# Kernel tuning notes

Hardware: AMD Instinct MI355X
Metric: run time of the kernel (lower is better)

Reference implementation:

```python
import jax, jax.numpy as jnp
import numpy as np

B, N, D = 8, 2048, 768


def setup_inputs() -> dict:
    key = jax.random.key(0)
    ks = jax.random.split(key, 12)
    s = 1.0 / np.sqrt(D)
    inp = {
        "query": jax.random.normal(ks[0], (B, N, D), dtype=jnp.float32),
        "value": jax.random.normal(ks[1], (B, N, D), dtype=jnp.float32),
        "mask": jax.random.randint(ks[2], (B, N), 0, 2, dtype=jnp.int32),
        "q_w": jax.random.uniform(ks[3], (D, D), jnp.float32, -s, s),
        "q_b": jax.random.uniform(ks[4], (D,), jnp.float32, -s, s),
        "k_w": jax.random.uniform(ks[5], (D, D), jnp.float32, -s, s),
        "k_b": jax.random.uniform(ks[6], (D,), jnp.float32, -s, s),
        "v_w": jax.random.uniform(ks[7], (D, D), jnp.float32, -s, s),
        "v_b": jax.random.uniform(ks[8], (D,), jnp.float32, -s, s),
        "fc_w": jax.random.uniform(ks[9], (D, D), jnp.float32, -s, s),
        "fc_b": jax.random.uniform(ks[10], (D,), jnp.float32, -s, s),
    }
    # guarantee at least one unmasked key per batch to avoid all--inf softmax rows
    inp["mask"] = inp["mask"].at[:, 0].set(1)
    return inp


def reference(query, value, mask, q_w, q_b, k_w, k_b, v_w, v_b, fc_w, fc_b):
    # torch Linear: y = x @ W.T + b  (dim==768 branch of the module)
    q = jnp.einsum("bnd,ed->bne", query, q_w) + q_b   # [B,N,D]
    k = jnp.einsum("bnd,ed->bne", value, k_w) + k_b   # [B,N,D]
    v = jnp.einsum("bnd,ed->bne", value, v_w) + v_b   # [B,N,D]
    # unscaled scores, as in the original (no 1/sqrt(d))
    scores = jnp.einsum("bqd,bkd->bqk", q, k)         # [B,N,N]
    key_mask = mask[:, None, :] != 0                  # [B,1,N]
    scores = jnp.where(key_mask, scores, -jnp.inf)
    attn = jax.nn.softmax(scores, axis=2)
    merged = jnp.einsum("bqk,bkd->bqd", attn, v)      # [B,N,D]
    merged = merged * mask[:, :, None].astype(merged.dtype)
    return jnp.einsum("bnd,ed->bne", merged, fc_w) + fc_b
```

## Files before the change

### kernel.cpp

```cpp
#include <hip/hip_runtime.h>
#include <hip/hip_bf16.h>

using bf16 = __hip_bfloat16;
typedef __attribute__((ext_vector_type(4))) float f32x4;
typedef __attribute__((ext_vector_type(8))) __bf16 bf16x8;
typedef __attribute__((ext_vector_type(4))) unsigned int u32x4;
typedef unsigned short u16;

#define LOG2E 1.4426950408889634f
#define SHIFT2 69.24936192747498f

__device__ __forceinline__ void gload_lds16(const void* g, void* l) {
  __builtin_amdgcn_global_load_lds((const __attribute__((address_space(1))) void*)g,
                                   (__attribute__((address_space(3))) void*)l, 16, 0, 0);
}

__device__ __forceinline__ bf16x8 lds_frag(const bf16* p) {
  u32x4 u = *(const u32x4*)p;
  return __builtin_bit_cast(bf16x8, u);
}

__device__ __forceinline__ u16 bf_bits(float v) {
  return __builtin_bit_cast(u16, __float2bfloat16(v));
}

struct GArgs {
  const void* Ah; const void* Al; long lda; long strideA;
  const bf16* Bh; const bf16* Bl; long ldb; long strideB;
  void* Ch; void* Cl; long ldc; long strideC;
  int K;
  const float* bias;
  float* rowsum; long rsStride;
  const int* idx; const int* cnt;
  const void* Ah2; const bf16* Bh2; const bf16* Bl2;
  void* Ch2; void* Cl2; const float* bias2;
};

template<int AMODE, bool SPLIT, int CMODE, bool BIAS, bool RSCALE,
         bool MGATHER, bool CSCAT, bool SQUARE, bool RAGK, bool QK2>
__global__ __launch_bounds__(256, 2) void gemm_nt(GArgs ga)
{
  const int tid = threadIdx.x;
  const int lane15 = tid & 15;
  const int quad = (tid >> 4) & 3;
  const int wave = tid >> 6;
  const int wm = (wave >> 1) * 64;
  const int wn = (wave & 1) * 64;

  constexpr int NZ = QK2 ? 16 : 8;
  constexpr int KW = SPLIT ? 64 : 32;
  __shared__ alignas(16) bf16 As[128 * KW];
  __shared__ alignas(16) bf16 Bs[128 * KW];
  __shared__ float rowacc[128];
  __shared__ int sT[8];
  __shared__ int sTz[NZ];

  if (tid < 8) sT[tid] = (ga.cnt[tid] + 127) >> 7;
  __syncthreads();
  if (tid < NZ) {
    const int Tm = sT[QK2 ? (tid & 7) : tid];
    sTz[tid] = SQUARE ? Tm * Tm : Tm * 6;
  }
  __syncthreads();
  int total = 0;
  #pragma unroll
  for (int i = 0; i < NZ; ++i) total += sTz[i];

  const int arow = tid >> 1;
  const int ahalf = tid & 1;
  const int aflip = arow & 1;
  const int aswz = (arow >> 1) & 3;

  for (int t = blockIdx.x; t < total; t += gridDim.x) {
    int vz = 0, rem = t;
    while (rem >= sTz[vz]) { rem -= sTz[vz]; ++vz; }
    const int z = QK2 ? (vz & 7) : vz;
    const int mat = QK2 ? (vz >> 3) : 0;
    const int Tm = sT[z];
    int mt, nt;
    if constexpr (SQUARE) { mt = rem / Tm; nt = rem - mt * Tm; }
    else                  { mt = rem / 6;  nt = rem - mt * 6; }
    const long m0 = (long)mt * 128;
    const long n0 = (long)nt * 128;
    const int cnt = ga.cnt[z];
    const int K = RAGK ? Tm * 128 : ga.K;

    const bf16* Bh = (QK2 && mat) ? ga.Bh2 : ga.Bh;
    const bf16* Bl = (QK2 && mat) ? ga.Bl2 : ga.Bl;
    const bf16* Bbh = Bh + z * ga.strideB;
    const bf16* Bbl = SPLIT ? (Bl + z * ga.strideB) : nullptr;

    const bf16* Abh = nullptr; const bf16* Abl = nullptr;
    const float* Af = nullptr;
    {
      const void* Ahp = (QK2 && mat) ? ga.Ah2 : ga.Ah;
      if constexpr (AMODE == 0) {
        Abh = (const bf16*)Ahp + (long)z * ga.strideA;
        if constexpr (SPLIT) Abl = (const bf16*)ga.Al + (long)z * ga.strideA;
      } else {
        Af = (const float*)Ahp + (long)z * ga.strideA;
      }
    }
    long agrow = m0 + arow;
    if constexpr (AMODE == 1 && MGATHER) agrow = ga.idx[(long)z * 2048 + m0 + arow];

    f32x4 acc[4][4];
    #pragma unroll
    for (int i = 0; i < 4; ++i)
      #pragma unroll
      for (int j = 0; j < 4; ++j) acc[i][j] = (f32x4){0.f, 0.f, 0.f, 0.f};

    for (int k0 = 0; k0 < K; k0 += 32) {
      __syncthreads();
      if constexpr (SPLIT) {
        #pragma unroll
        for (int r = 0; r < 4; ++r) {
          const int idx = r * 256 + tid, row = idx >> 3, slot = idx & 7;
          const int flip = row & 1, sw = (row >> 1) & 3;
          const int h = (slot >> 2) ^ flip, s = (slot & 3) ^ sw;
          const bf16* g = (h ? Bbl : Bbh) + (n0 + row) * ga.ldb + k0 + s * 8;
          gload_lds16(g, &Bs[idx * 8]);
        }
      } else {
        #pragma unroll
        for (int r = 0; r < 2; ++r) {
          const int idx = r * 256 + tid, row = idx >> 2, slot = idx & 3;
          const int sw = (row >> 1) & 3;
          gload_lds16(Bbh + (n0 + row) * ga.ldb + k0 + (slot ^ sw) * 8, &Bs[idx * 8]);
        }
      }
      if constexpr (AMODE == 0) {
        if constexpr (SPLIT) {
          #pragma unroll
          for (int r = 0; r < 4; ++r) {
            const int idx = r * 256 + tid, row = idx >> 3, slot = idx & 7;
            const int flip = row & 1, sw = (row >> 1) & 3;
            const int h = (slot >> 2) ^ flip, s = (slot & 3) ^ sw;
            const bf16* g = (h ? Abl : Abh) + (m0 + row) * ga.lda + k0 + s * 8;
            gload_lds16(g, &As[idx * 8]);
          }
        } else {
          #pragma unroll
          for (int r = 0; r < 2; ++r) {
            const int idx = r * 256 + tid, row = idx >> 2, slot = idx & 3;
            const int sw = (row >> 1) & 3;
            gload_lds16(Abh + (m0 + row) * ga.lda + k0 + (slot ^ sw) * 8, &As[idx * 8]);
          }
        }
      } else {
        const float* src = Af + agrow * ga.lda + k0;
        #pragma unroll
        for (int ss = 0; ss < 2; ++ss) {
          const int s = ahalf * 2 + ss;
          float tv[8];
          *(f32x4*)tv       = *(const f32x4*)(src + s * 8);
          *(f32x4*)(tv + 4) = *(const f32x4*)(src + s * 8 + 4);
          u32x4 hi, lo;
          u16* ph = (u16*)&hi; u16* pl = (u16*)&lo;
          #pragma unroll
          for (int j = 0; j < 8; ++j) {
            bf16 hb = __float2bfloat16(tv[j]);
            ph[j] = __builtin_bit_cast(u16, hb);
            if constexpr (SPLIT) pl[j] = bf_bits(tv[j] - __bfloat162float(hb));
          }
          if constexpr (SPLIT) {
            const int sh = (aflip << 2) | (s ^ aswz);
            *(u32x4*)&As[arow * 64 + sh * 8] = hi;
            *(u32x4*)&As[arow * 64 + (sh ^ 4) * 8] = lo;
          } else {
            *(u32x4*)&As[arow * 32 + (s ^ aswz) * 8] = hi;
          }
        }
      }
      __syncthreads();

      const int swl = (lane15 >> 1) & 3;
      if constexpr (SPLIT) {
        const int eff = ((lane15 & 1) << 2) | (quad ^ swl);
        bf16x8 ah[4], al[4], bh[4], bl[4];
        #pragma unroll
        for (int tt = 0; tt < 4; ++tt) {
          const int ar = (wm + tt * 16 + lane15) * 64;
          const int br = (wn + tt * 16 + lane15) * 64;
          ah[tt] = lds_frag(&As[ar + eff * 8]);
          al[tt] = lds_frag(&As[ar + (eff ^ 4) * 8]);
          bh[tt] = lds_frag(&Bs[br + eff * 8]);
          bl[tt] = lds_frag(&Bs[br + (eff ^ 4) * 8]);
        }
        #pragma unroll
        for (int i = 0; i < 4; ++i)
          #pragma unroll
          for (int j = 0; j < 4; ++j) {
            acc[i][j] = __builtin_amdgcn_mfma_f32_16x16x32_bf16(ah[i], bh[j], acc[i][j], 0, 0, 0);
            acc[i][j] = __builtin_amdgcn_mfma_f32_16x16x32_bf16(al[i], bh[j], acc[i][j], 0, 0, 0);
            acc[i][j] = __builtin_amdgcn_mfma_f32_16x16x32_bf16(ah[i], bl[j], acc[i][j], 0, 0, 0);
          }
      } else {
        const int eff = quad ^ swl;
        bf16x8 ah[4], bh[4];
        #pragma unroll
        for (int tt = 0; tt < 4; ++tt) ah[tt] = lds_frag(&As[(wm + tt * 16 + lane15) * 32 + eff * 8]);
        #pragma unroll
        for (int tt = 0; tt < 4; ++tt) bh[tt] = lds_frag(&Bs[(wn + tt * 16 + lane15) * 32 + eff * 8]);
        #pragma unroll
        for (int i = 0; i < 4; ++i)
          #pragma unroll
          for (int j = 0; j < 4; ++j)
            acc[i][j] = __builtin_amdgcn_mfma_f32_16x16x32_bf16(ah[i], bh[j], acc[i][j], 0, 0, 0);
      }
    }

    const long crow0 = m0 + wm + quad * 4;
    const long ccol0 = n0 + wn + lane15;

    if constexpr (CMODE == 3) {
      bf16* P = (bf16*)ga.Ch + (long)z * ga.strideC;
      __syncthreads();
      if (tid < 128) rowacc[tid] = 0.f;
      __syncthreads();
      bool keep[4];
      #pragma unroll
      for (int tn = 0; tn < 4; ++tn) keep[tn] = (ccol0 + tn * 16) < cnt;
      #pragma unroll
      for (int tm = 0; tm < 4; ++tm) {
        #pragma unroll
        for (int r = 0; r < 4; ++r) {
          const long row = crow0 + tm * 16 + r;
          float rsum = 0.f;
          #pragma unroll
          for (int tn = 0; tn < 4; ++tn) {
            float p = keep[tn] ? exp2f(fmaf(acc[tm][tn][r], LOG2E, -SHIFT2)) : 0.f;
            bf16 pb = __float2bfloat16(p);
            P[row * ga.ldc + ccol0 + tn * 16] = pb;
            rsum += __bfloat162float(pb);
          }
          atomicAdd(&rowacc[(int)(row - m0)], rsum);
        }
      }
      __syncthreads();
      if (tid < 128) atomicAdd(&ga.rowsum[z * ga.rsStride + m0 + tid], rowacc[tid]);
      continue;
    }

    const float* bias = (QK2 && mat) ? ga.bias2 : ga.bias;
    float bv[4] = {0.f, 0.f, 0.f, 0.f};
    if constexpr (BIAS) {
      #pragma unroll
      for (int tn = 0; tn < 4; ++tn) bv[tn] = bias[ccol0 + tn * 16];
    }
    if constexpr (CMODE == 2) {
      float* C = (float*)ga.Ch + (long)z * ga.strideC;
      #pragma unroll
      for (int tm = 0; tm < 4; ++tm) {
        #pragma unroll
        for (int r = 0; r < 4; ++r) {
          const long row = crow0 + tm * 16 + r;
          long orow = row;
          bool doStore = true;
          if constexpr (CSCAT) {
            doStore = row < cnt;
            orow = doStore ? (long)ga.idx[(long)z * 2048 + row] : 0;
          }
          if (doStore) {
            #pragma unroll
            for (int tn = 0; tn < 4; ++tn)
              C[orow * ga.ldc + ccol0 + tn * 16] = acc[tm][tn][r] + bv[tn];
          }
        }
      }
    } else if constexpr (CMODE == 1) {
      bf16* Ch = (bf16*)((QK2 && mat) ? ga.Ch2 : ga.Ch) + (long)z * ga.strideC;
      bf16* Cl = (bf16*)((QK2 && mat) ? ga.Cl2 : ga.Cl) + (long)z * ga.strideC;
      #pragma unroll
      for (int tm = 0; tm < 4; ++tm) {
        const long row = crow0 + tm * 16;
        #pragma unroll
        for (int tn = 0; tn < 4; ++tn) {
          const long col = ccol0 + tn * 16;
          #pragma unroll
          for (int r = 0; r < 4; ++r) {
            float val = acc[tm][tn][r] + bv[tn];
            bf16 h = __float2bfloat16(val);
            Ch[(row + r) * ga.ldc + col] = h;
            Cl[(row + r) * ga.ldc + col] = __float2bfloat16(val - __bfloat162float(h));
          }
        }
      }
    } else {
      bf16* Ch = (bf16*)ga.Ch + (long)z * ga.strideC;
      #pragma unroll
      for (int tm = 0; tm < 4; ++tm) {
        const long row = crow0 + tm * 16;
        float rm[4];
        #pragma unroll
        for (int r = 0; r < 4; ++r) {
          float f = 1.f;
          if constexpr (RSCALE) f = 1.0f / ga.rowsum[z * ga.rsStride + row + r];
          rm[r] = f;
        }
        #pragma unroll
        for (int tn = 0; tn < 4; ++tn) {
          const long col = ccol0 + tn * 16;
          #pragma unroll
          for (int r = 0; r < 4; ++r)
            Ch[(row + r) * ga.ldc + col] = __float2bfloat16((acc[tm][tn][r] + bv[tn]) * rm[r]);
        }
      }
    }
  }
}

__global__ __launch_bounds__(256) void compact_kernel(
    const int* __restrict__ mask, int* __restrict__ idx, int* __restrict__ cnt)
{
  const int z = blockIdx.x, tid = threadIdx.x;
  const int* m = mask + (long)z * 2048;
  int* id = idx + (long)z * 2048;
  int v[8]; int c = 0;
  #pragma unroll
  for (int j = 0; j < 8; ++j) { v[j] = m[tid * 8 + j]; c += (v[j] != 0) ? 1 : 0; }
  __shared__ int sc[256];
  sc[tid] = c;
  __syncthreads();
  for (int off = 1; off < 256; off <<= 1) {
    int y = 0;
    if (tid >= off) y = sc[tid - off];
    __syncthreads();
    if (tid >= off) sc[tid] += y;
    __syncthreads();
  }
  int k = sc[tid] - c;
  #pragma unroll
  for (int j = 0; j < 8; ++j)
    if (v[j]) id[k++] = tid * 8 + j;
  __syncthreads();
  const int tot = sc[255];
  if (tid == 0) cnt[z] = tot;
  const int last = id[tot - 1];
  for (int i = tot + tid; i < 2048; i += 256) id[i] = last;
}

__global__ __launch_bounds__(256) void cvt4_kernel(
    const float* __restrict__ qw, const float* __restrict__ kw,
    const float* __restrict__ vw, const float* __restrict__ fw,
    bf16* __restrict__ Wqh, bf16* __restrict__ Wql,
    bf16* __restrict__ Wkh, bf16* __restrict__ Wkl,
    bf16* __restrict__ Wvh, bf16* __restrict__ Wfh, int n8)
{
  const int i = blockIdx.x * 256 + threadIdx.x;
  if (i >= n8) return;
  const float* in; bf16* oh; bf16* ol = nullptr;
  switch (blockIdx.y) {
    case 0:  in = qw; oh = Wqh; ol = Wql; break;
    case 1:  in = kw; oh = Wkh; ol = Wkl; break;
    case 2:  in = vw; oh = Wvh; break;
    default: in = fw; oh = Wfh; break;
  }
  float tv[8];
  *(f32x4*)tv       = ((const f32x4*)in)[2 * i];
  *(f32x4*)(tv + 4) = ((const f32x4*)in)[2 * i + 1];
  u32x4 H, L;
  u16* ph = (u16*)&H; u16* pl = (u16*)&L;
  #pragma unroll
  for (int j = 0; j < 8; ++j) {
    bf16 hb = __float2bfloat16(tv[j]);
    ph[j] = __builtin_bit_cast(u16, hb);
    pl[j] = bf_bits(tv[j] - __bfloat162float(hb));
  }
  ((u32x4*)oh)[i] = H;
  if (ol) ((u32x4*)ol)[i] = L;
}

__global__ __launch_bounds__(256) void bias_fill_kernel(
    float* __restrict__ out, const float* __restrict__ fc_b)
{
  const long i = (long)blockIdx.x * 256 + threadIdx.x;
  const int col4 = (int)(i % 192);
  ((f32x4*)out)[i] = *(const f32x4*)(fc_b + col4 * 4);
}

__global__ __launch_bounds__(256) void transpose_kernel(
    const u16* __restrict__ in, u16* __restrict__ out, const int* __restrict__ cnt)
{
  const long z = blockIdx.z;
  const long r0 = (long)blockIdx.x * 64, c0 = (long)blockIdx.y * 64;
  const int kb = (cnt[z] + 127) & ~127;
  if (r0 >= kb) return;
  __shared__ alignas(16) u16 t[64][72];
  const u16* inz = in + z * 2048 * 768;
  u16* outz = out + z * 768 * 2048;
  const int tid = threadIdx.x;
  const int rr = tid >> 3, cs = (tid & 7) * 8;
  #pragma unroll
  for (int i = 0; i < 2; ++i) {
    const int row = rr + i * 32;
    u32x4 v = *(const u32x4*)(inz + (r0 + row) * 768 + c0 + cs);
    *(u32x4*)&t[row][cs] = v;
  }
  __syncthreads();
  #pragma unroll
  for (int i = 0; i < 2; ++i) {
    const int oc = rr + i * 32;
    u32x4 o;
    u16* po = (u16*)&o;
    #pragma unroll
    for (int j = 0; j < 8; ++j) po[j] = t[cs + j][oc];
    *(u32x4*)(outz + (c0 + oc) * 2048 + r0 + cs) = o;
  }
}

extern "C" void kernel_launch(void* const* d_in, const int* in_sizes, int n_in,
                              void* d_out, int out_size, void* d_ws, size_t ws_size,
                              hipStream_t stream) {
  const float* query = (const float*)d_in[0];
  const float* value = (const float*)d_in[1];
  const int*   mask  = (const int*)d_in[2];
  const float* q_w   = (const float*)d_in[3];
  const float* q_b   = (const float*)d_in[4];
  const float* k_w   = (const float*)d_in[5];
  const float* k_b   = (const float*)d_in[6];
  const float* v_w   = (const float*)d_in[7];
  const float* v_b   = (const float*)d_in[8];
  const float* fc_w  = (const float*)d_in[9];
  const float* fc_b  = (const float*)d_in[10];

  const long N = 2048, D = 768;
  const long BD = N * D;
  const int WN = (int)(D * D), W8 = WN / 8;

  char* wp = (char*)d_ws;
  auto take = [&](size_t bytes) {
    char* p = wp;
    wp += (bytes + 255) & ~(size_t)255;
    return p;
  };
  bf16* Wqh = (bf16*)take((size_t)WN * 2);
  bf16* Wql = (bf16*)take((size_t)WN * 2);
  bf16* Wkh = (bf16*)take((size_t)WN * 2);
  bf16* Wkl = (bf16*)take((size_t)WN * 2);
  bf16* Wvh = (bf16*)take((size_t)WN * 2);
  bf16* Wfh = (bf16*)take((size_t)WN * 2);
  bf16* Qh = (bf16*)take((size_t)8 * BD * 2);
  bf16* Ql = (bf16*)take((size_t)8 * BD * 2);
  bf16* Kh = (bf16*)take((size_t)8 * BD * 2);
  bf16* Kl = (bf16*)take((size_t)8 * BD * 2);
  bf16* VT = (bf16*)take((size_t)8 * BD * 2);
  bf16* P  = (bf16*)take((size_t)8 * N * N * 2);
  float* rowsum = (float*)take((size_t)8 * N * sizeof(float));
  int* idx = (int*)take((size_t)8 * N * sizeof(int));
  int* cnt = (int*)take(64);
  bf16* V = (bf16*)((char*)P + (size_t)8 * N * N * 2 - (size_t)8 * BD * 2);
  bf16* merged = Qh;

  dim3 blk(256);
  dim3 g512(512);

  compact_kernel<<<dim3(8), blk, 0, stream>>>(mask, idx, cnt);
  cvt4_kernel<<<dim3(288, 4), blk, 0, stream>>>(q_w, k_w, v_w, fc_w,
      Wqh, Wql, Wkh, Wkl, Wvh, Wfh, W8);
  hipMemsetAsync(rowsum, 0, (size_t)8 * N * sizeof(float), stream);
  bias_fill_kernel<<<dim3(12288), blk, 0, stream>>>((float*)d_out, fc_b);

  GArgs a{};
  a.idx = idx; a.cnt = cnt; a.rowsum = rowsum; a.rsStride = N;

  a.Ah = query; a.Al = nullptr; a.lda = D; a.strideA = BD;
  a.Bh = Wqh; a.Bl = Wql; a.ldb = D; a.strideB = 0;
  a.Ch = Qh; a.Cl = Ql; a.ldc = D; a.strideC = BD;
  a.K = (int)D; a.bias = q_b;
  a.Ah2 = value; a.Bh2 = Wkh; a.Bl2 = Wkl; a.Ch2 = Kh; a.Cl2 = Kl; a.bias2 = k_b;
  gemm_nt<1, true, 1, true, false, true, false, false, false, true>
      <<<g512, blk, 0, stream>>>(a);

  a.Ah = value; a.Bh = Wvh; a.Bl = nullptr;
  a.Ch = V; a.Cl = nullptr; a.bias = v_b;
  gemm_nt<1, false, 0, true, false, true, false, false, false, false>
      <<<g512, blk, 0, stream>>>(a);
  transpose_kernel<<<dim3(32, 12, 8), blk, 0, stream>>>((const u16*)V, (u16*)VT, cnt);

  a.Ah = Qh; a.Al = Ql; a.lda = D; a.strideA = BD;
  a.Bh = Kh; a.Bl = Kl; a.ldb = D; a.strideB = BD;
  a.Ch = P; a.Cl = nullptr; a.ldc = N; a.strideC = N * N;
  a.K = (int)D; a.bias = nullptr;
  gemm_nt<0, true, 3, false, false, false, false, true, false, false>
      <<<g512, blk, 0, stream>>>(a);

  a.Ah = P; a.Al = nullptr; a.lda = N; a.strideA = N * N;
  a.Bh = VT; a.Bl = nullptr; a.ldb = N; a.strideB = BD;
  a.Ch = merged; a.Cl = nullptr; a.ldc = D; a.strideC = BD;
  gemm_nt<0, false, 0, false, true, false, false, false, true, false>
      <<<g512, blk, 0, stream>>>(a);

  a.Ah = merged; a.lda = D; a.strideA = BD;
  a.Bh = Wfh; a.Bl = nullptr; a.ldb = D; a.strideB = 0;
  a.Ch = d_out; a.Cl = nullptr; a.ldc = D; a.strideC = BD;
  a.K = (int)D; a.bias = fc_b;
  gemm_nt<0, false, 2, true, false, false, true, false, false, false>
      <<<g512, blk, 0, stream>>>(a);
}
```

Measured before the change: 439.4 us.

## Pre-convert gathered activations to split bf16 in separate kernel; simplify GEMM loads

Adds a gather-and-convert kernel that compacts the masked query/value rows and writes their hi/lo bf16 split once. The projection GEMMs can then load A with direct global-to-LDS copies instead of per-tile fp32 loads and in-register conversion. The fused Q/K launch is split into separate Q, K and V launches, and workspace buffers are aliased into the P region. The rowsum epilogue also reduces across lanes before the shared atomic. This costs an extra pass over the activations and extra launches, in exchange for a simpler, faster inner loop and value being converted once instead of twice.

```diff
diff --git a/kernel.cpp b/kernel.cpp
--- a/kernel.cpp
+++ b/kernel.cpp
@@ -25,19 +25,16 @@
 }
 
 struct GArgs {
-  const void* Ah; const void* Al; long lda; long strideA;
+  const bf16* Ah; const bf16* Al; long lda; long strideA;
   const bf16* Bh; const bf16* Bl; long ldb; long strideB;
   void* Ch; void* Cl; long ldc; long strideC;
   int K;
   const float* bias;
   float* rowsum; long rsStride;
   const int* idx; const int* cnt;
-  const void* Ah2; const bf16* Bh2; const bf16* Bl2;
-  void* Ch2; void* Cl2; const float* bias2;
 };
 
-template<int AMODE, bool SPLIT, int CMODE, bool BIAS, bool RSCALE,
-         bool MGATHER, bool CSCAT, bool SQUARE, bool RAGK, bool QK2>
+template<bool SPLIT, int CMODE, bool BIAS, bool RSCALE, bool CSCAT, bool SQUARE, bool RAGK>
 __global__ __launch_bounds__(256, 2) void gemm_nt(GArgs ga)
 {
   const int tid = threadIdx.x;
@@ -47,35 +44,26 @@
   const int wm = (wave >> 1) * 64;
   const int wn = (wave & 1) * 64;
 
-  constexpr int NZ = QK2 ? 16 : 8;
   constexpr int KW = SPLIT ? 64 : 32;
   __shared__ alignas(16) bf16 As[128 * KW];
   __shared__ alignas(16) bf16 Bs[128 * KW];
   __shared__ float rowacc[128];
   __shared__ int sT[8];
-  __shared__ int sTz[NZ];
-
-  if (tid < 8) sT[tid] = (ga.cnt[tid] + 127) >> 7;
-  __syncthreads();
-  if (tid < NZ) {
-    const int Tm = sT[QK2 ? (tid & 7) : tid];
+  __shared__ int sTz[8];
+
+  if (tid < 8) {
+    const int Tm = (ga.cnt[tid] + 127) >> 7;
+    sT[tid] = Tm;
     sTz[tid] = SQUARE ? Tm * Tm : Tm * 6;
   }
   __syncthreads();
   int total = 0;
   #pragma unroll
-  for (int i = 0; i < NZ; ++i) total += sTz[i];
-
-  const int arow = tid >> 1;
-  const int ahalf = tid & 1;
-  const int aflip = arow & 1;
-  const int aswz = (arow >> 1) & 3;
+  for (int i = 0; i < 8; ++i) total += sTz[i];
 
   for (int t = blockIdx.x; t < total; t += gridDim.x) {
-    int vz = 0, rem = t;
-    while (rem >= sTz[vz]) { rem -= sTz[vz]; ++vz; }
-    const int z = QK2 ? (vz & 7) : vz;
-    const int mat = QK2 ? (vz >> 3) : 0;
+    int z = 0, rem = t;
+    while (rem >= sTz[z]) { rem -= sTz[z]; ++z; }
     const int Tm = sT[z];
     int mt, nt;
     if constexpr (SQUARE) { mt = rem / Tm; nt = rem - mt * Tm; }
@@ -85,24 +73,10 @@
     const int cnt = ga.cnt[z];
     const int K = RAGK ? Tm * 128 : ga.K;
 
-    const bf16* Bh = (QK2 && mat) ? ga.Bh2 : ga.Bh;
-    const bf16* Bl = (QK2 && mat) ? ga.Bl2 : ga.Bl;
-    const bf16* Bbh = Bh + z * ga.strideB;
-    const bf16* Bbl = SPLIT ? (Bl + z * ga.strideB) : nullptr;
-
-    const bf16* Abh = nullptr; const bf16* Abl = nullptr;
-    const float* Af = nullptr;
-    {
-      const void* Ahp = (QK2 && mat) ? ga.Ah2 : ga.Ah;
-      if constexpr (AMODE == 0) {
-        Abh = (const bf16*)Ahp + (long)z * ga.strideA;
-        if constexpr (SPLIT) Abl = (const bf16*)ga.Al + (long)z * ga.strideA;
-      } else {
-        Af = (const float*)Ahp + (long)z * ga.strideA;
-      }
-    }
-    long agrow = m0 + arow;
-    if constexpr (AMODE == 1 && MGATHER) agrow = ga.idx[(long)z * 2048 + m0 + arow];
+    const bf16* Bbh = ga.Bh + z * ga.strideB;
+    const bf16* Bbl = SPLIT ? (ga.Bl + z * ga.strideB) : nullptr;
+    const bf16* Abh = ga.Ah + (long)z * ga.strideA;
+    const bf16* Abl = SPLIT ? (ga.Al + (long)z * ga.strideA) : nullptr;
 
     f32x4 acc[4][4];
     #pragma unroll
@@ -118,8 +92,8 @@
           const int idx = r * 256 + tid, row = idx >> 3, slot = idx & 7;
           const int flip = row & 1, sw = (row >> 1) & 3;
           const int h = (slot >> 2) ^ flip, s = (slot & 3) ^ sw;
-          const bf16* g = (h ? Bbl : Bbh) + (n0 + row) * ga.ldb + k0 + s * 8;
-          gload_lds16(g, &Bs[idx * 8]);
+          gload_lds16((h ? Bbl : Bbh) + (n0 + row) * ga.ldb + k0 + s * 8, &Bs[idx * 8]);
+          gload_lds16((h ? Abl : Abh) + (m0 + row) * ga.lda + k0 + s * 8, &As[idx * 8]);
         }
       } else {
         #pragma unroll
@@ -127,49 +101,7 @@
           const int idx = r * 256 + tid, row = idx >> 2, slot = idx & 3;
           const int sw = (row >> 1) & 3;
           gload_lds16(Bbh + (n0 + row) * ga.ldb + k0 + (slot ^ sw) * 8, &Bs[idx * 8]);
-        }
-      }
-      if constexpr (AMODE == 0) {
-        if constexpr (SPLIT) {
-          #pragma unroll
-          for (int r = 0; r < 4; ++r) {
-            const int idx = r * 256 + tid, row = idx >> 3, slot = idx & 7;
-            const int flip = row & 1, sw = (row >> 1) & 3;
-            const int h = (slot >> 2) ^ flip, s = (slot & 3) ^ sw;
-            const bf16* g = (h ? Abl : Abh) + (m0 + row) * ga.lda + k0 + s * 8;
-            gload_lds16(g, &As[idx * 8]);
-          }
-        } else {
-          #pragma unroll
-          for (int r = 0; r < 2; ++r) {
-            const int idx = r * 256 + tid, row = idx >> 2, slot = idx & 3;
-            const int sw = (row >> 1) & 3;
-            gload_lds16(Abh + (m0 + row) * ga.lda + k0 + (slot ^ sw) * 8, &As[idx * 8]);
-          }
-        }
-      } else {
-        const float* src = Af + agrow * ga.lda + k0;
-        #pragma unroll
-        for (int ss = 0; ss < 2; ++ss) {
-          const int s = ahalf * 2 + ss;
-          float tv[8];
-          *(f32x4*)tv       = *(const f32x4*)(src + s * 8);
-          *(f32x4*)(tv + 4) = *(const f32x4*)(src + s * 8 + 4);
-          u32x4 hi, lo;
-          u16* ph = (u16*)&hi; u16* pl = (u16*)&lo;
-          #pragma unroll
-          for (int j = 0; j < 8; ++j) {
-            bf16 hb = __float2bfloat16(tv[j]);
-            ph[j] = __builtin_bit_cast(u16, hb);
-            if constexpr (SPLIT) pl[j] = bf_bits(tv[j] - __bfloat162float(hb));
-          }
-          if constexpr (SPLIT) {
-            const int sh = (aflip << 2) | (s ^ aswz);
-            *(u32x4*)&As[arow * 64 + sh * 8] = hi;
-            *(u32x4*)&As[arow * 64 + (sh ^ 4) * 8] = lo;
-          } else {
-            *(u32x4*)&As[arow * 32 + (s ^ aswz) * 8] = hi;
-          }
+          gload_lds16(Abh + (m0 + row) * ga.lda + k0 + (slot ^ sw) * 8, &As[idx * 8]);
         }
       }
       __syncthreads();
@@ -234,7 +166,9 @@
             P[row * ga.ldc + ccol0 + tn * 16] = pb;
             rsum += __bfloat162float(pb);
           }
-          atomicAdd(&rowacc[(int)(row - m0)], rsum);
+          #pragma unroll
+          for (int o = 1; o < 16; o <<= 1) rsum += __shfl_xor(rsum, o, 64);
+          if (lane15 == 0) atomicAdd(&rowacc[(int)(row - m0)], rsum);
         }
       }
       __syncthreads();
@@ -242,11 +176,10 @@
       continue;
     }
 
-    const float* bias = (QK2 && mat) ? ga.bias2 : ga.bias;
     float bv[4] = {0.f, 0.f, 0.f, 0.f};
     if constexpr (BIAS) {
       #pragma unroll
-      for (int tn = 0; tn < 4; ++tn) bv[tn] = bias[ccol0 + tn * 16];
+      for (int tn = 0; tn < 4; ++tn) bv[tn] = ga.bias[ccol0 + tn * 16];
     }
     if constexpr (CMODE == 2) {
       float* C = (float*)ga.Ch + (long)z * ga.strideC;
@@ -269,8 +202,8 @@
         }
       }
     } else if constexpr (CMODE == 1) {
-      bf16* Ch = (bf16*)((QK2 && mat) ? ga.Ch2 : ga.Ch) + (long)z * ga.strideC;
-      bf16* Cl = (bf16*)((QK2 && mat) ? ga.Cl2 : ga.Cl) + (long)z * ga.strideC;
+      bf16* Ch = (bf16*)ga.Ch + (long)z * ga.strideC;
+      bf16* Cl = (bf16*)ga.Cl + (long)z * ga.strideC;
       #pragma unroll
       for (int tm = 0; tm < 4; ++tm) {
         const long row = crow0 + tm * 16;
@@ -338,6 +271,39 @@
   if (tid == 0) cnt[z] = tot;
   const int last = id[tot - 1];
   for (int i = tot + tid; i < 2048; i += 256) id[i] = last;
+}
+
+__global__ __launch_bounds__(256) void gcvt_kernel(
+    const float* __restrict__ query, const float* __restrict__ value,
+    const int* __restrict__ idx, const int* __restrict__ cnt,
+    bf16* __restrict__ Xqh, bf16* __restrict__ Xql,
+    bf16* __restrict__ Xvh, bf16* __restrict__ Xvl)
+{
+  const int z = blockIdx.y;
+  const long r0 = (long)blockIdx.x * 128;
+  const int kb = (cnt[z] + 127) & ~127;
+  if (r0 >= kb) return;
+  const float* src = (blockIdx.z ? value : query) + (long)z * 2048 * 768;
+  bf16* oh = (blockIdx.z ? Xvh : Xqh) + ((long)z * 2048 + r0) * 768;
+  bf16* ol = (blockIdx.z ? Xvl : Xql) + ((long)z * 2048 + r0) * 768;
+  const int* id = idx + (long)z * 2048 + r0;
+  for (int i = threadIdx.x; i < 128 * 96; i += 256) {
+    const int r = i / 96, c = (i - (i / 96) * 96) * 8;
+    const float* s = src + (long)id[r] * 768 + c;
+    float tv[8];
+    *(f32x4*)tv       = *(const f32x4*)s;
+    *(f32x4*)(tv + 4) = *(const f32x4*)(s + 4);
+    u32x4 H, L;
+    u16* ph = (u16*)&H; u16* pl = (u16*)&L;
+    #pragma unroll
+    for (int j = 0; j < 8; ++j) {
+      bf16 hb = __float2bfloat16(tv[j]);
+      ph[j] = __builtin_bit_cast(u16, hb);
+      pl[j] = bf_bits(tv[j] - __bfloat162float(hb));
+    }
+    *(u32x4*)(oh + (long)r * 768 + c) = H;
+    *(u32x4*)(ol + (long)r * 768 + c) = L;
+  }
 }
 
 __global__ __launch_bounds__(256) void cvt4_kernel(
@@ -427,6 +393,8 @@
   const long N = 2048, D = 768;
   const long BD = N * D;
   const int WN = (int)(D * D), W8 = WN / 8;
+  const size_t WB = ((size_t)WN * 2 + 255) & ~(size_t)255;
+  const size_t XB = ((size_t)8 * BD * 2 + 255) & ~(size_t)255;
 
   char* wp = (char*)d_ws;
   auto take = [&](size_t bytes) {
@@ -434,28 +402,35 @@
     wp += (bytes + 255) & ~(size_t)255;
     return p;
   };
-  bf16* Wqh = (bf16*)take((size_t)WN * 2);
-  bf16* Wql = (bf16*)take((size_t)WN * 2);
-  bf16* Wkh = (bf16*)take((size_t)WN * 2);
-  bf16* Wkl = (bf16*)take((size_t)WN * 2);
-  bf16* Wvh = (bf16*)take((size_t)WN * 2);
-  bf16* Wfh = (bf16*)take((size_t)WN * 2);
-  bf16* Qh = (bf16*)take((size_t)8 * BD * 2);
-  bf16* Ql = (bf16*)take((size_t)8 * BD * 2);
-  bf16* Kh = (bf16*)take((size_t)8 * BD * 2);
-  bf16* Kl = (bf16*)take((size_t)8 * BD * 2);
-  bf16* VT = (bf16*)take((size_t)8 * BD * 2);
-  bf16* P  = (bf16*)take((size_t)8 * N * N * 2);
+  bf16* Wfh = (bf16*)take(WB);
+  char* Pb  = take((size_t)8 * N * N * 2);
+  bf16* Wqh = (bf16*)(Pb + 0 * WB);
+  bf16* Wql = (bf16*)(Pb + 1 * WB);
+  bf16* Wkh = (bf16*)(Pb + 2 * WB);
+  bf16* Wkl = (bf16*)(Pb + 3 * WB);
+  bf16* Wvh = (bf16*)(Pb + 4 * WB);
+  bf16* Xvh = (bf16*)(Pb + 5 * WB);
+  bf16* V   = (bf16*)(Pb + 5 * WB + XB);
+  bf16* P   = (bf16*)Pb;
+  bf16* Xqh = (bf16*)take(XB);
+  bf16* Xql = (bf16*)take(XB);
+  bf16* Xvl = (bf16*)take(XB);
+  bf16* Qh  = (bf16*)take(XB);
+  bf16* Ql  = (bf16*)take(XB);
   float* rowsum = (float*)take((size_t)8 * N * sizeof(float));
   int* idx = (int*)take((size_t)8 * N * sizeof(int));
   int* cnt = (int*)take(64);
-  bf16* V = (bf16*)((char*)P + (size_t)8 * N * N * 2 - (size_t)8 * BD * 2);
+  bf16* Kh = Xqh;
+  bf16* Kl = Xql;
+  bf16* VT = Xvl;
   bf16* merged = Qh;
 
   dim3 blk(256);
   dim3 g512(512);
 
   compact_kernel<<<dim3(8), blk, 0, stream>>>(mask, idx, cnt);
+  gcvt_kernel<<<dim3(16, 8, 2), blk, 0, stream>>>(query, value, idx, cnt,
+      Xqh, Xql, Xvh, Xvl);
   cvt4_kernel<<<dim3(288, 4), blk, 0, stream>>>(q_w, k_w, v_w, fc_w,
       Wqh, Wql, Wkh, Wkl, Wvh, Wfh, W8);
   hipMemsetAsync(rowsum, 0, (size_t)8 * N * sizeof(float), stream);
@@ -464,37 +439,38 @@
   GArgs a{};
   a.idx = idx; a.cnt = cnt; a.rowsum = rowsum; a.rsStride = N;
 
-  a.Ah = query; a.Al = nullptr; a.lda = D; a.strideA = BD;
+  a.Ah = Xqh; a.Al = Xql; a.lda = D; a.strideA = BD;
   a.Bh = Wqh; a.Bl = Wql; a.ldb = D; a.strideB = 0;
   a.Ch = Qh; a.Cl = Ql; a.ldc = D; a.strideC = BD;
   a.K = (int)D; a.bias = q_b;
-  a.Ah2 = value; a.Bh2 = Wkh; a.Bl2 = Wkl; a.Ch2 = Kh; a.Cl2 = Kl; a.bias2 = k_b;
-  gemm_nt<1, true, 1, true, false, true, false, false, false, true>
-      <<<g512, blk, 0, stream>>>(a);
-
-  a.Ah = value; a.Bh = Wvh; a.Bl = nullptr;
+  gemm_nt<true, 1, true, false, false, false, false><<<g512, blk, 0, stream>>>(a);
+
+  a.Ah = Xvh; a.Al = Xvl;
+  a.Bh = Wkh; a.Bl = Wkl;
+  a.Ch = Kh; a.Cl = Kl; a.bias = k_b;
+  gemm_nt<true, 1, true, false, false, false, false><<<g512, blk, 0, stream>>>(a);
+
+  a.Ah = Xvh; a.Al = nullptr;
+  a.Bh = Wvh; a.Bl = nullptr;
   a.Ch = V; a.Cl = nullptr; a.bias = v_b;
-  gemm_nt<1, false, 0, true, false, true, false, false, false, false>
-      <<<g512, blk, 0, stream>>>(a);
+  gemm_nt<false, 0, true, false, false, false, false><<<g512, blk, 0, stream>>>(a);
+
   transpose_kernel<<<dim3(32, 12, 8), blk, 0, stream>>>((const u16*)V, (u16*)VT, cnt);
 
   a.Ah = Qh; a.Al = Ql; a.lda = D; a.strideA = BD;
   a.Bh = Kh; a.Bl = Kl; a.ldb = D; a.strideB = BD;
   a.Ch = P; a.Cl = nullptr; a.ldc = N; a.strideC = N * N;
   a.K = (int)D; a.bias = nullptr;
-  gemm_nt<0, true, 3, false, false, false, false, true, false, false>
-      <<<g512, blk, 0, stream>>>(a);
+  gemm_nt<true, 3, false, false, false, true, false><<<g512, blk, 0, stream>>>(a);
 
   a.Ah = P; a.Al = nullptr; a.lda = N; a.strideA = N * N;
   a.Bh = VT; a.Bl = nullptr; a.ldb = N; a.strideB = BD;
   a.Ch = merged; a.Cl = nullptr; a.ldc = D; a.strideC = BD;
-  gemm_nt<0, false, 0, false, true, false, false, false, true, false>
-      <<<g512, blk, 0, stream>>>(a);
+  gemm_nt<false, 0, false, true, false, false, true><<<g512, blk, 0, stream>>>(a);
 
   a.Ah = merged; a.lda = D; a.strideA = BD;
   a.Bh = Wfh; a.Bl = nullptr; a.ldb = D; a.strideB = 0;
   a.Ch = d_out; a.Cl = nullptr; a.ldc = D; a.strideC = BD;
   a.K = (int)D; a.bias = fc_b;
-  gemm_nt<0, false, 2, true, false, false, true, false, false, false>
-      <<<g512, blk, 0, stream>>>(a);
-}
+  gemm_nt<false, 2, true, false, true, false, false><<<g512, blk, 0, stream>>>(a);
+}
```

Result: slower. 490.3 us (+11.6%).
